# Optimization experiments

Measured on AMD Instinct MI355X. Metric: run time of the kernel, lower is better.

The kernel has to match this reference:

```python
import jax, jax.numpy as jnp
import numpy as np

D = 1024      # input_size / d_model
H = 16        # num_heads
HD = D // H   # head_size = 64
T = 2048      # block_size / seq_len
B = 2
FF = 4 * D
EPS = 1e-5


def setup_inputs() -> dict:
    key = jax.random.key(0)
    ks = jax.random.split(key, 16)
    s_in = 1.0 / np.sqrt(D)
    s_ff = 1.0 / np.sqrt(FF)
    return {
        "x": jax.random.normal(ks[0], (B, T, D), dtype=jnp.float32),
        # per-head unbiased projections, stacked over heads: [H, D, HD]
        "wq": jax.random.normal(ks[1], (H, D, HD), dtype=jnp.float32) * s_in,
        "wk": jax.random.normal(ks[2], (H, D, HD), dtype=jnp.float32) * s_in,
        "wv": jax.random.normal(ks[3], (H, D, HD), dtype=jnp.float32) * s_in,
        "w_proj": jax.random.normal(ks[4], (D, D), dtype=jnp.float32) * s_in,
        "b_proj": jnp.zeros((D,), dtype=jnp.float32),
        "ln1_g": jnp.ones((D,), dtype=jnp.float32),
        "ln1_b": jnp.zeros((D,), dtype=jnp.float32),
        "ln2_g": jnp.ones((D,), dtype=jnp.float32),
        "ln2_b": jnp.zeros((D,), dtype=jnp.float32),
        "w1": jax.random.normal(ks[5], (D, FF), dtype=jnp.float32) * s_in,
        "b1": jnp.zeros((FF,), dtype=jnp.float32),
        "w2": jax.random.normal(ks[6], (FF, D), dtype=jnp.float32) * s_ff,
        "b2": jnp.zeros((D,), dtype=jnp.float32),
    }


def _layernorm(x, g, b):
    mu = jnp.mean(x, axis=-1, keepdims=True)
    var = jnp.mean(jnp.square(x - mu), axis=-1, keepdims=True)
    return (x - mu) * jax.lax.rsqrt(var + EPS) * g + b


def reference(x, wq, wk, wv, w_proj, b_proj, ln1_g, ln1_b, ln2_g, ln2_b, w1, b1, w2, b2):
    Bv, Tv, _ = x.shape
    h = _layernorm(x, ln1_g, ln1_b)                       # [B,T,D]
    q = jnp.einsum("btc,hcd->bhtd", h, wq)
    k = jnp.einsum("btc,hcd->bhtd", h, wk)
    v = jnp.einsum("btc,hcd->bhtd", h, wv)
    scores = jnp.einsum("bhtd,bhsd->bhts", q, k) * (HD ** -0.5)  # [B,H,T,T]
    causal = jnp.tril(jnp.ones((Tv, Tv), dtype=bool))
    scores = jnp.where(causal, scores, -jnp.inf)
    attn = jax.nn.softmax(scores, axis=-1)
    out = jnp.einsum("bhts,bhsd->bhtd", attn, v)          # [B,H,T,HD]
    out = out.transpose(0, 2, 1, 3).reshape(Bv, Tv, H * HD)  # concat heads
    out = out @ w_proj + b_proj
    x = x + out
    h2 = _layernorm(x, ln2_g, ln2_b)
    ff = jax.nn.gelu(h2 @ w1 + b1, approximate=False) @ w2 + b2
    return x + ff
```

## Files before the change

### kernel.cpp

```cpp
#include <hip/hip_runtime.h>
#include <hip/hip_bf16.h>
#include <cstdint>
#include <cstddef>
#include <math.h>

#define D_ 1024
#define H_ 16
#define HD_ 64
#define T_ 2048
#define B_ 2
#define FF_ 4096
#define BT_ (B_*T_)
#define NT_ 32

typedef unsigned short u16;
typedef __attribute__((ext_vector_type(8))) __bf16 bf16x8;
typedef __attribute__((ext_vector_type(8))) u16 u16x8;
typedef __attribute__((ext_vector_type(4))) float f32x4;

__device__ __forceinline__ u16 f2bf(float f) {
  unsigned u = __builtin_bit_cast(unsigned, f);
  u += 0x7FFFu + ((u >> 16) & 1u);
  return (u16)(u >> 16);
}

__device__ __forceinline__ unsigned cvt_pk_bf16(float a, float b) {
  unsigned r;
  asm("v_cvt_pk_bf16_f32 %0, %1, %2" : "=v"(r) : "v"(a), "v"(b));
  return r;
}

__device__ __forceinline__ void gload16(const void* g, void* l) {
  __builtin_amdgcn_global_load_lds((__attribute__((address_space(1))) void*)g,
                                   (__attribute__((address_space(3))) void*)l, 16, 0, 0);
}

__global__ __launch_bounds__(256) void transpose_w(const float* __restrict__ in,
                                                   u16* __restrict__ out, int R, int C) {
  __shared__ float tile[32][33];
  const int z = blockIdx.z;
  const float* inz = in + (size_t)z * R * C;
  const int x = blockIdx.x * 32 + threadIdx.x;
  const int y0 = blockIdx.y * 32 + threadIdx.y;
  #pragma unroll
  for (int j = 0; j < 32; j += 8)
    tile[threadIdx.y + j][threadIdx.x] = inz[(size_t)(y0 + j) * C + x];
  __syncthreads();
  const int orr = blockIdx.y * 32 + threadIdx.x;
  const int oc0 = blockIdx.x * 32 + threadIdx.y;
  u16* outz = out + (size_t)z * C * R;
  #pragma unroll
  for (int j = 0; j < 32; j += 8)
    outz[(size_t)(oc0 + j) * R + orr] = f2bf(tile[threadIdx.x][threadIdx.y + j]);
}

__global__ __launch_bounds__(256) void ln_rows(const float* __restrict__ x,
    const float* __restrict__ g, const float* __restrict__ bb, u16* __restrict__ out) {
  const int row = blockIdx.x, tid = threadIdx.x;
  const float4 v = ((const float4*)(x + (size_t)row * D_))[tid];
  float s = v.x + v.y + v.z + v.w;
  float sq = v.x*v.x + v.y*v.y + v.z*v.z + v.w*v.w;
  #pragma unroll
  for (int m = 1; m < 64; m <<= 1) { s += __shfl_xor(s, m); sq += __shfl_xor(sq, m); }
  __shared__ float ss[4], qs[4];
  if ((tid & 63) == 0) { ss[tid >> 6] = s; qs[tid >> 6] = sq; }
  __syncthreads();
  s  = ss[0] + ss[1] + ss[2] + ss[3];
  sq = qs[0] + qs[1] + qs[2] + qs[3];
  const float mean = s * (1.f / D_);
  const float var  = sq * (1.f / D_) - mean * mean;
  const float rstd = rsqrtf(var + 1e-5f);
  const float4 gv = ((const float4*)g)[tid];
  const float4 bv = ((const float4*)bb)[tid];
  u16 o[4];
  o[0] = f2bf((v.x - mean) * rstd * gv.x + bv.x);
  o[1] = f2bf((v.y - mean) * rstd * gv.y + bv.y);
  o[2] = f2bf((v.z - mean) * rstd * gv.z + bv.z);
  o[3] = f2bf((v.w - mean) * rstd * gv.w + bv.w);
  *(ushort4*)(out + (size_t)row * D_ + tid * 4) = *(ushort4*)o;
}

template<int ACT, int BIAS, int OUTBF, int PARTIAL>
__global__ __launch_bounds__(512, 1) void gemm256(
    const u16* __restrict__ A, const u16* __restrict__ Bt,
    const float* __restrict__ bias, const float* resid,
    void* Cout, int M, int N, int K, int Kper) {
  __shared__ __attribute__((aligned(16))) u16 LA[2][256 * 64];
  __shared__ __attribute__((aligned(16))) u16 LB[2][256 * 64];

  const int tid = threadIdx.x;
  const int wid = tid >> 6, lane = tid & 63;
  const int wr = wid >> 2, wc = wid & 3;
  const int frow = lane & 15, hi = lane >> 4;

  const int gx = gridDim.x;
  const int nwg = gx * gridDim.y;
  const int orig = blockIdx.y * gx + blockIdx.x;
  const int cpx = nwg >> 3;
  const int swz = (orig & 7) * cpx + (orig >> 3);
  const int bm = (swz / gx) * 256, bn = (swz % gx) * 256;
  const int z = PARTIAL ? blockIdx.z : 0;
  const int koff = z * Kper;
  const int nt = Kper >> 6;

  const u16* Atile = A + (size_t)bm * K + koff;
  const u16* Btile = Bt + (size_t)bn * K + koff;

  const int lr = lane >> 3, lc = lane & 7;
  const int gch = lc ^ lr;

  f32x4 acc[8][4] = {};

  #define STAGE(kt, db)                                                          \
    {                                                                            \
      const u16* ga = Atile + (kt) * 64;                                         \
      const u16* gb = Btile + (kt) * 64;                                         \
      u16* la = &LA[db][0];                                                      \
      u16* lb = &LB[db][0];                                                      \
      _Pragma("unroll")                                                          \
      for (int j = 0; j < 4; j++) {                                              \
        const int rw = j * 64 + wid * 8;                                         \
        gload16(ga + (size_t)(rw + lr) * K + gch * 8, la + rw * 64);             \
        gload16(gb + (size_t)(rw + lr) * K + gch * 8, lb + rw * 64);             \
      }                                                                          \
    }

  STAGE(0, 0);

  for (int t = 0; t < nt; ++t) {
    if (t + 1 < nt) {
      STAGE(t + 1, (t + 1) & 1);
      asm volatile("s_waitcnt vmcnt(8)" ::: "memory");
    } else {
      asm volatile("s_waitcnt vmcnt(0)" ::: "memory");
    }
    __builtin_amdgcn_s_barrier();

    const u16* Ab = &LA[t & 1][0];
    const u16* Bb = &LB[t & 1][0];

    bf16x8 bfr[4][2];
    #pragma unroll
    for (int ni = 0; ni < 4; ni++)
      #pragma unroll
      for (int ks = 0; ks < 2; ks++) {
        const int row = wc * 64 + ni * 16 + frow;
        bfr[ni][ks] = *(const bf16x8*)(Bb + row * 64 + (((ks * 4 + hi) ^ (row & 7)) << 3));
      }
    #pragma unroll
    for (int q = 0; q < 4; q++) {
      bf16x8 af[2][2];
      #pragma unroll
      for (int m2 = 0; m2 < 2; m2++)
        #pragma unroll
        for (int ks = 0; ks < 2; ks++) {
          const int row = wr * 128 + (q * 2 + m2) * 16 + frow;
          af[m2][ks] = *(const bf16x8*)(Ab + row * 64 + (((ks * 4 + hi) ^ (row & 7)) << 3));
        }
      __builtin_amdgcn_s_setprio(1);
      #pragma unroll
      for (int m2 = 0; m2 < 2; m2++)
        #pragma unroll
        for (int ni = 0; ni < 4; ni++)
          #pragma unroll
          for (int ks = 0; ks < 2; ks++)
            acc[q * 2 + m2][ni] =
                __builtin_amdgcn_mfma_f32_16x16x32_bf16(af[m2][ks], bfr[ni][ks],
                                                        acc[q * 2 + m2][ni], 0, 0, 0);
      __builtin_amdgcn_s_setprio(0);
    }
    __builtin_amdgcn_s_barrier();
  }
  #undef STAGE

  const int r0 = bm + wr * 128 + hi * 4;
  const int c0 = bn + wc * 64 + frow;
  #pragma unroll
  for (int mi = 0; mi < 8; mi++) {
    #pragma unroll
    for (int ni = 0; ni < 4; ni++) {
      #pragma unroll
      for (int r = 0; r < 4; r++) {
        float v = acc[mi][ni][r];
        const int rr = r0 + mi * 16 + r;
        const int cc = c0 + ni * 16;
        if (PARTIAL) {
          ((float*)Cout)[((size_t)z * M + rr) * N + cc] = v;
        } else {
          if (BIAS) v += bias[cc];
          if (ACT == 1) v = 0.5f * v * (1.0f + erff(v * 0.70710678118f));
          if (resid) v += resid[(size_t)rr * N + cc];
          if (OUTBF) ((u16*)Cout)[(size_t)rr * N + cc] = f2bf(v);
          else       ((float*)Cout)[(size_t)rr * N + cc] = v;
        }
      }
    }
  }
}

template<int NPART>
__global__ __launch_bounds__(256) void reduce_parts(
    const float* __restrict__ parts, const float* __restrict__ bias,
    const float* __restrict__ resid, float* __restrict__ out, int MN, int N) {
  const int i4 = (blockIdx.x * 256 + threadIdx.x) * 4;
  if (i4 >= MN) return;
  float4 s = *(const float4*)(parts + i4);
  #pragma unroll
  for (int p = 1; p < NPART; p++) {
    const float4 t = *(const float4*)(parts + (size_t)p * MN + i4);
    s.x += t.x; s.y += t.y; s.z += t.z; s.w += t.w;
  }
  const float4 bv = *(const float4*)(bias + (i4 & (N - 1)));
  const float4 rv = *(const float4*)(resid + i4);
  s.x += bv.x + rv.x; s.y += bv.y + rv.y; s.z += bv.z + rv.z; s.w += bv.w + rv.w;
  *(float4*)(out + i4) = s;
}

__global__ __launch_bounds__(256) void reduce2_ln(
    const float* __restrict__ parts, const float* __restrict__ bias,
    const float* __restrict__ resid, const float* __restrict__ g,
    const float* __restrict__ bb, float* __restrict__ xout,
    u16* __restrict__ h2, int MN) {
  const int row = blockIdx.x, tid = threadIdx.x;
  const int i4 = row * D_ + tid * 4;
  float4 s = *(const float4*)(parts + i4);
  const float4 t = *(const float4*)(parts + (size_t)MN + i4);
  const float4 bv = *(const float4*)(bias + tid * 4);
  const float4 rv = *(const float4*)(resid + i4);
  s.x += t.x + bv.x + rv.x; s.y += t.y + bv.y + rv.y;
  s.z += t.z + bv.z + rv.z; s.w += t.w + bv.w + rv.w;
  *(float4*)(xout + i4) = s;
  float sm = s.x + s.y + s.z + s.w;
  float sq = s.x*s.x + s.y*s.y + s.z*s.z + s.w*s.w;
  #pragma unroll
  for (int m = 1; m < 64; m <<= 1) { sm += __shfl_xor(sm, m); sq += __shfl_xor(sq, m); }
  __shared__ float ss[4], qs[4];
  if ((tid & 63) == 0) { ss[tid >> 6] = sm; qs[tid >> 6] = sq; }
  __syncthreads();
  sm = ss[0] + ss[1] + ss[2] + ss[3];
  sq = qs[0] + qs[1] + qs[2] + qs[3];
  const float mean = sm * (1.f / D_);
  const float var  = sq * (1.f / D_) - mean * mean;
  const float rstd = rsqrtf(var + 1e-5f);
  const float4 gv = ((const float4*)g)[tid];
  const float4 b2v = ((const float4*)bb)[tid];
  u16 o[4];
  o[0] = f2bf((s.x - mean) * rstd * gv.x + b2v.x);
  o[1] = f2bf((s.y - mean) * rstd * gv.y + b2v.y);
  o[2] = f2bf((s.z - mean) * rstd * gv.z + b2v.z);
  o[3] = f2bf((s.w - mean) * rstd * gv.w + b2v.w);
  *(ushort4*)(h2 + (size_t)row * D_ + tid * 4) = *(ushort4*)o;
}

__global__ __launch_bounds__(256) void repack_qkv(const u16* __restrict__ qkv,
    u16* __restrict__ q, u16* __restrict__ k, u16* __restrict__ vt) {
  const int t0 = blockIdx.x * 64, bh = blockIdx.y;
  const int b = bh >> 4, h = bh & 15;
  const int tid = threadIdx.x;
  const int c = (tid & 7) * 8;
  __shared__ __attribute__((aligned(16))) u16 vs[64][72];
  #pragma unroll
  for (int p = 0; p < 2; p++) {
    const int tl = p * 32 + (tid >> 3);
    const size_t inrow = ((size_t)b * T_ + t0 + tl) * 3072 + h * 64;
    u16x8 qv = *(const u16x8*)(qkv + inrow + c);
    bf16x8 kv = *(const bf16x8*)(qkv + inrow + 1024 + c);
    bf16x8 vv = *(const bf16x8*)(qkv + inrow + 2048 + c);
    alignas(16) u16 qs[8];
    #pragma unroll
    for (int e = 0; e < 8; e++) {
      const float f = __builtin_bit_cast(float, ((unsigned)qv[e]) << 16) * 0.18033688011112042f;
      qs[e] = f2bf(f);
    }
    *(u16x8*)(q + ((size_t)bh * T_ + t0 + tl) * HD_ + c) = *(u16x8*)qs;
    *(bf16x8*)(k + ((size_t)bh * T_ + t0 + tl) * HD_ + c) = kv;
    *(bf16x8*)&vs[tl][c] = vv;
  }
  __syncthreads();
  const int d = tid >> 2, tc = (tid & 3) * 16;
  alignas(16) u16 tmp[16];
  #pragma unroll
  for (int j = 0; j < 16; j++) tmp[j] = vs[tc + j][d];
  *(bf16x8*)(vt + ((size_t)bh * HD_ + d) * T_ + t0 + tc)     = *(bf16x8*)&tmp[0];
  *(bf16x8*)(vt + ((size_t)bh * HD_ + d) * T_ + t0 + tc + 8) = *(bf16x8*)&tmp[8];
}

__global__ __launch_bounds__(512) void attn_fwd(
    const u16* __restrict__ q, const u16* __restrict__ k,
    const u16* __restrict__ vt, u16* __restrict__ out) {
  __shared__ __attribute__((aligned(16))) u16 Ps[8][16 * 64];
  __shared__ __attribute__((aligned(16))) u16 Kb[2][64 * 64];
  __shared__ __attribute__((aligned(16))) u16 Vb[2][64 * 64];

  const int bid = blockIdx.x;
  const int xcd = bid & 7, j = bid >> 3;
  const int bh  = xcd + 8 * (j & 3);
  const int qb  = 15 - (j >> 2);
  const int b = bh >> 4, h = bh & 15;
  const int tid = threadIdx.x, wid = tid >> 6, lane = tid & 63;
  const u16* kh = k  + (size_t)bh * T_ * HD_;
  const u16* vh = vt + (size_t)bh * HD_ * T_;
  const int q0 = qb * 128;
  const int nkt = 2 * qb + 2;
  const int wlast = 2 * qb + (wid >> 2);

  const int frow = lane & 15;
  const int hi   = lane >> 4;
  const int fk   = hi * 8;
  const int rowb = hi * 4;
  const int colb = frow;
  const int srow = tid >> 3;
  const int gch  = (tid & 7) ^ (srow & 7);

  u16x8 onebits = (u16x8)((u16)0x3F80);
  bf16x8 b_one = (frow == 0) ? __builtin_bit_cast(bf16x8, onebits) : (bf16x8){};

  u16* Pw = &Ps[wid][0];

  const u16* qrow = q + ((size_t)bh * T_ + q0 + wid * 16 + frow) * HD_;
  bf16x8 aq[2];
  aq[0] = *(const bf16x8*)(qrow + fk);
  aq[1] = *(const bf16x8*)(qrow + 32 + fk);

  float m2[4] = {-3e38f, -3e38f, -3e38f, -3e38f};
  f32x4 acc_l = {};
  f32x4 acc_o[4] = {};

  int cur = 0;
  gload16(kh + (size_t)srow * HD_ + gch * 8, &Kb[0][(wid * 8) * 64]);
  gload16(vh + (size_t)srow * T_ + gch * 8,  &Vb[0][(wid * 8) * 64]);
  __syncthreads();

  for (int kt = 0; kt < nkt; ++kt) {
    if (kt + 1 < nkt) {
      const int nx = cur ^ 1, ktn = kt + 1;
      gload16(kh + (size_t)(ktn * 64 + srow) * HD_ + gch * 8, &Kb[nx][(wid * 8) * 64]);
      gload16(vh + (size_t)srow * T_ + ktn * 64 + gch * 8,    &Vb[nx][(wid * 8) * 64]);
    }

    if (kt <= wlast) {
      const u16* Kc = &Kb[cur][0];
      const u16* Vc = &Vb[cur][0];

      float p2[4][4];
      __builtin_amdgcn_s_setprio(1);
      #pragma unroll
      for (int ni = 0; ni < 4; ni++) {
        f32x4 s = {};
        #pragma unroll
        for (int ks = 0; ks < 2; ks++) {
          const int row = ni * 16 + frow;
          const int ch  = ks * 4 + hi;
          bf16x8 bk = *(const bf16x8*)(Kc + row * 64 + ((ch ^ (row & 7)) << 3));
          s = __builtin_amdgcn_mfma_f32_16x16x32_bf16(aq[ks], bk, s, 0, 0, 0);
        }
        #pragma unroll
        for (int r = 0; r < 4; r++) p2[ni][r] = s[r];
      }
      __builtin_amdgcn_s_setprio(0);

      if (kt >= nkt - 2) {
        #pragma unroll
        for (int ni = 0; ni < 4; ni++)
          #pragma unroll
          for (int r = 0; r < 4; r++) {
            const bool msk = (kt * 64 + ni * 16 + colb) > (q0 + wid * 16 + rowb + r);
            if (msk) p2[ni][r] = -3e38f;
          }
      }

      float lmax[4];
      #pragma unroll
      for (int r = 0; r < 4; r++)
        lmax[r] = fmaxf(fmaxf(p2[0][r], p2[1][r]), fmaxf(p2[2][r], p2[3][r]));
      int ok = 1;
      #pragma unroll
      for (int r = 0; r < 4; r++) ok &= (lmax[r] <= m2[r] + 8.0f);
      if (!__all(ok)) {
        #pragma unroll
        for (int r = 0; r < 4; r++) {
          float rm = lmax[r];
          rm = fmaxf(rm, __shfl_xor(rm, 1));
          rm = fmaxf(rm, __shfl_xor(rm, 2));
          rm = fmaxf(rm, __shfl_xor(rm, 4));
          rm = fmaxf(rm, __shfl_xor(rm, 8));
          const float mnew = fmaxf(m2[r], rm);
          const float corr = exp2f(m2[r] - mnew);
          m2[r] = mnew;
          acc_l[r] *= corr;
          #pragma unroll
          for (int ni = 0; ni < 4; ni++) acc_o[ni][r] *= corr;
        }
      }
      #pragma unroll
      for (int ni = 0; ni < 4; ni++)
        #pragma unroll
        for (int r = 0; r < 4; r++) p2[ni][r] = exp2f(p2[ni][r] - m2[r]);

      #pragma unroll
      for (int ni = 0; ni < 4; ni++) {
        #pragma unroll
        for (int r = 0; r < 4; r += 2) {
          const unsigned pk = cvt_pk_bf16(p2[ni][r], p2[ni][r + 1]);
          const int lr0 = rowb + r, lr1 = rowb + r + 1;
          const int ch = ni * 2 + (colb >> 3);
          Pw[lr0 * 64 + ((ch ^ (lr0 & 7)) << 3) + (colb & 7)] = (u16)pk;
          Pw[lr1 * 64 + ((ch ^ (lr1 & 7)) << 3) + (colb & 7)] = (u16)(pk >> 16);
        }
      }
      bf16x8 ap[2];
      {
        const int c0 = (0 * 4 + hi) ^ (frow & 7);
        const int c1 = (1 * 4 + hi) ^ (frow & 7);
        ap[0] = *(const bf16x8*)(Pw + frow * 64 + (c0 << 3));
        ap[1] = *(const bf16x8*)(Pw + frow * 64 + (c1 << 3));
      }

      __builtin_amdgcn_s_setprio(1);
      #pragma unroll
      for (int ks = 0; ks < 2; ks++)
        acc_l = __builtin_amdgcn_mfma_f32_16x16x32_bf16(ap[ks], b_one, acc_l, 0, 0, 0);
      #pragma unroll
      for (int ni = 0; ni < 4; ni++) {
        #pragma unroll
        for (int ks = 0; ks < 2; ks++) {
          const int row = ni * 16 + frow;
          const int ch  = ks * 4 + hi;
          bf16x8 bv = *(const bf16x8*)(Vc + row * 64 + ((ch ^ (row & 7)) << 3));
          acc_o[ni] = __builtin_amdgcn_mfma_f32_16x16x32_bf16(ap[ks], bv, acc_o[ni], 0, 0, 0);
        }
      }
      __builtin_amdgcn_s_setprio(0);
    }

    __syncthreads();
    cur ^= 1;
  }

  float linv[4];
  #pragma unroll
  for (int r = 0; r < 4; r++) {
    const float lv = __shfl(acc_l[r], lane & 48);
    linv[r] = 1.0f / lv;
  }
  #pragma unroll
  for (int ni = 0; ni < 4; ni++)
    #pragma unroll
    for (int r = 0; r < 4; r++) {
      const float ov = acc_o[ni][r] * linv[r];
      const size_t row = (size_t)b * T_ + q0 + wid * 16 + rowb + r;
      out[row * D_ + h * HD_ + ni * 16 + colb] = f2bf(ov);
    }
}

extern "C" void kernel_launch(void* const* d_in, const int* in_sizes, int n_in,
                              void* d_out, int out_size, void* d_ws, size_t ws_size,
                              hipStream_t stream) {
  (void)in_sizes; (void)n_in; (void)out_size; (void)ws_size;
  const float* x      = (const float*)d_in[0];
  const float* wq     = (const float*)d_in[1];
  const float* wk     = (const float*)d_in[2];
  const float* wv     = (const float*)d_in[3];
  const float* w_proj = (const float*)d_in[4];
  const float* b_proj = (const float*)d_in[5];
  const float* ln1_g  = (const float*)d_in[6];
  const float* ln1_b  = (const float*)d_in[7];
  const float* ln2_g  = (const float*)d_in[8];
  const float* ln2_b  = (const float*)d_in[9];
  const float* w1     = (const float*)d_in[10];
  const float* b1     = (const float*)d_in[11];
  const float* w2     = (const float*)d_in[12];
  const float* b2     = (const float*)d_in[13];

  uint8_t* ws = (uint8_t*)d_ws;
  const size_t MB = 1024 * 1024;
  u16* wqkv_t = (u16*)(ws + 0);
  u16* wproj_t = (u16*)(ws + 6 * MB);
  u16* w1t  = (u16*)(ws + 8 * MB);
  u16* w2t  = (u16*)(ws + 16 * MB);
  u16* hbuf = (u16*)(ws + 24 * MB);
  u16* qkv  = (u16*)(ws + 32 * MB);
  u16* qb   = (u16*)(ws + 56 * MB);
  u16* kb   = (u16*)(ws + 64 * MB);
  u16* vtb  = (u16*)(ws + 72 * MB);
  u16* aout = (u16*)(ws + 80 * MB);
  u16* h2   = (u16*)(ws + 88 * MB);
  u16* ff1  = (u16*)(ws + 96 * MB);
  float* pparts = (float*)(ws + 32 * MB);
  float* fparts = (float*)(ws + 32 * MB);
  float* xout = (float*)d_out;

  const dim3 tb(32, 8);
  transpose_w<<<dim3(HD_/32, D_/32, H_), tb, 0, stream>>>(wq, wqkv_t, D_, HD_);
  transpose_w<<<dim3(HD_/32, D_/32, H_), tb, 0, stream>>>(wk, wqkv_t + (size_t)D_*D_, D_, HD_);
  transpose_w<<<dim3(HD_/32, D_/32, H_), tb, 0, stream>>>(wv, wqkv_t + 2*(size_t)D_*D_, D_, HD_);
  transpose_w<<<dim3(D_/32, D_/32, 1),  tb, 0, stream>>>(w_proj, wproj_t, D_, D_);
  transpose_w<<<dim3(FF_/32, D_/32, 1), tb, 0, stream>>>(w1, w1t, D_, FF_);
  transpose_w<<<dim3(D_/32, FF_/32, 1), tb, 0, stream>>>(w2, w2t, FF_, D_);

  ln_rows<<<BT_, 256, 0, stream>>>(x, ln1_g, ln1_b, hbuf);

  gemm256<0,0,1,0><<<dim3(3072/256, BT_/256), 512, 0, stream>>>(
      hbuf, wqkv_t, nullptr, nullptr, qkv, BT_, 3072, D_, D_);

  repack_qkv<<<dim3(T_/64, B_*H_), 256, 0, stream>>>(qkv, qb, kb, vtb);

  attn_fwd<<<dim3(512), 512, 0, stream>>>(qb, kb, vtb, aout);

  gemm256<0,0,0,1><<<dim3(D_/256, BT_/256, 2), 512, 0, stream>>>(
      aout, wproj_t, nullptr, nullptr, pparts, BT_, D_, D_, D_/2);
  reduce2_ln<<<BT_, 256, 0, stream>>>(
      pparts, b_proj, x, ln2_g, ln2_b, xout, h2, BT_*D_);

  gemm256<1,1,1,0><<<dim3(FF_/256, BT_/256), 512, 0, stream>>>(
      h2, w1t, b1, nullptr, ff1, BT_, FF_, D_, D_);

  gemm256<0,0,0,1><<<dim3(D_/256, BT_/256, 4), 512, 0, stream>>>(
      ff1, w2t, nullptr, nullptr, fparts, BT_, D_, FF_, FF_/4);
  reduce_parts<4><<<(BT_*D_)/1024, 256, 0, stream>>>(
      fparts, b2, xout, xout, BT_*D_, D_);
}
```

Measured before the change: 276.5 us.

## Interleave next-tile global-to-LDS loads across MFMA phases in GEMM main loop

Splits the staging of the next K-tile into four quarter-loads (two B halves, two A halves) that are issued one per compute phase inside the inner loop, instead of issuing all loads at the top of each iteration. Fine-grained vmcnt waits and barriers per phase let global loads overlap with MFMA work across the whole iteration. This adds more barriers per K-step and relies on careful vmcnt accounting, which risks stalls or races if the counts are wrong.

```diff
diff --git a/kernel.cpp b/kernel.cpp
--- a/kernel.cpp
+++ b/kernel.cpp
@@ -106,57 +106,65 @@
   const u16* Atile = A + (size_t)bm * K + koff;
   const u16* Btile = Bt + (size_t)bn * K + koff;
 
-  const int lr = lane >> 3, lc = lane & 7;
-  const int gch = lc ^ lr;
+  const int srow = tid >> 3;
+  const int gch  = (tid & 7) ^ (srow & 7);
 
   f32x4 acc[8][4] = {};
 
-  #define STAGE(kt, db)                                                          \
-    {                                                                            \
-      const u16* ga = Atile + (kt) * 64;                                         \
-      const u16* gb = Btile + (kt) * 64;                                         \
-      u16* la = &LA[db][0];                                                      \
-      u16* lb = &LB[db][0];                                                      \
-      _Pragma("unroll")                                                          \
-      for (int j = 0; j < 4; j++) {                                              \
-        const int rw = j * 64 + wid * 8;                                         \
-        gload16(ga + (size_t)(rw + lr) * K + gch * 8, la + rw * 64);             \
-        gload16(gb + (size_t)(rw + lr) * K + gch * 8, lb + rw * 64);             \
-      }                                                                          \
-    }
-
-  STAGE(0, 0);
-
-  for (int t = 0; t < nt; ++t) {
-    if (t + 1 < nt) {
-      STAGE(t + 1, (t + 1) & 1);
-      asm volatile("s_waitcnt vmcnt(8)" ::: "memory");
-    } else {
-      asm volatile("s_waitcnt vmcnt(0)" ::: "memory");
-    }
-    __builtin_amdgcn_s_barrier();
-
-    const u16* Ab = &LA[t & 1][0];
-    const u16* Bb = &LB[t & 1][0];
-
+  auto stageB = [&](int kt, int h, int db) {
+    #pragma unroll
+    for (int j = 0; j < 2; j++) {
+      const int rl = h * 128 + j * 64;
+      gload16(Btile + (size_t)(rl + srow) * K + (size_t)kt * 64 + gch * 8,
+              &LB[db][(rl + wid * 8) * 64]);
+    }
+  };
+  auto stageA = [&](int kt, int u, int db) {
+    #pragma unroll
+    for (int j = 0; j < 2; j++) {
+      const int rl = j * 128 + u * 64;
+      gload16(Atile + (size_t)(rl + srow) * K + (size_t)kt * 64 + gch * 8,
+              &LA[db][(rl + wid * 8) * 64]);
+    }
+  };
+
+  stageB(0, 0, 0); stageB(0, 1, 0); stageA(0, 0, 0); stageA(0, 1, 0);
+  asm volatile("s_waitcnt vmcnt(2)" ::: "memory");
+  __builtin_amdgcn_s_barrier();
+
+  for (int kt = 0; kt < nt; ++kt) {
+    const int db = kt & 1;
+    const u16* Ab = &LA[db][0];
+    const u16* Bb = &LB[db][0];
     bf16x8 bfr[4][2];
     #pragma unroll
-    for (int ni = 0; ni < 4; ni++)
-      #pragma unroll
-      for (int ks = 0; ks < 2; ks++) {
-        const int row = wc * 64 + ni * 16 + frow;
-        bfr[ni][ks] = *(const bf16x8*)(Bb + row * 64 + (((ks * 4 + hi) ^ (row & 7)) << 3));
-      }
-    #pragma unroll
-    for (int q = 0; q < 4; q++) {
+    for (int p = 0; p < 4; ++p) {
+      if (p == 0) {
+        #pragma unroll
+        for (int ni = 0; ni < 4; ni++)
+          #pragma unroll
+          for (int ks = 0; ks < 2; ks++) {
+            const int row = wc * 64 + ni * 16 + frow;
+            bfr[ni][ks] = *(const bf16x8*)(Bb + row * 64 + (((ks * 4 + hi) ^ (row & 7)) << 3));
+          }
+      }
       bf16x8 af[2][2];
       #pragma unroll
       for (int m2 = 0; m2 < 2; m2++)
         #pragma unroll
         for (int ks = 0; ks < 2; ks++) {
-          const int row = wr * 128 + (q * 2 + m2) * 16 + frow;
+          const int row = wr * 128 + (p * 2 + m2) * 16 + frow;
           af[m2][ks] = *(const bf16x8*)(Ab + row * 64 + (((ks * 4 + hi) ^ (row & 7)) << 3));
         }
+      if (kt + 1 < nt) {
+        if      (p == 0) stageB(kt + 1, 0, db ^ 1);
+        else if (p == 1) stageB(kt + 1, 1, db ^ 1);
+        else if (p == 2) stageA(kt + 1, 0, db ^ 1);
+        else             stageA(kt + 1, 1, db ^ 1);
+      }
+      __builtin_amdgcn_s_barrier();
+      asm volatile("s_waitcnt lgkmcnt(0)" ::: "memory");
+      __builtin_amdgcn_sched_barrier(0);
       __builtin_amdgcn_s_setprio(1);
       #pragma unroll
       for (int m2 = 0; m2 < 2; m2++)
@@ -164,14 +172,15 @@
         for (int ni = 0; ni < 4; ni++)
           #pragma unroll
           for (int ks = 0; ks < 2; ks++)
-            acc[q * 2 + m2][ni] =
+            acc[p * 2 + m2][ni] =
                 __builtin_amdgcn_mfma_f32_16x16x32_bf16(af[m2][ks], bfr[ni][ks],
-                                                        acc[q * 2 + m2][ni], 0, 0, 0);
+                                                        acc[p * 2 + m2][ni], 0, 0, 0);
       __builtin_amdgcn_s_setprio(0);
-    }
-    __builtin_amdgcn_s_barrier();
+      if (p == 1) asm volatile("s_waitcnt vmcnt(4)" ::: "memory");
+      if (p == 3) asm volatile("s_waitcnt vmcnt(2)" ::: "memory");
+      __builtin_amdgcn_s_barrier();
+    }
   }
-  #undef STAGE
 
   const int r0 = bm + wr * 128 + hi * 4;
   const int c0 = bn + wc * 64 + frow;
```

After: 267.1 us. 1.04x faster.
